# Performance work log

Hardware: AMD Instinct MI355X
Metric: run time of the kernel (lower is better)

The kernel has to match this reference:

```python
import jax, jax.numpy as jnp
import numpy as np

B, S, D, H = 2, 2048, 1024, 16
HD = D // H


def setup_inputs() -> dict:
    key = jax.random.key(0)
    ks = jax.random.split(key, 6)
    std = 1.0 / np.sqrt(D)
    return {
        "hidden_states": jax.random.normal(ks[0], (B, S, D), dtype=jnp.float32),
        "attention_mask": jnp.zeros((B, 1, S, S), dtype=jnp.float32),
        "Wq": jax.random.normal(ks[1], (D, D), dtype=jnp.float32) * std,
        "bq": jnp.zeros((D,), dtype=jnp.float32),
        "Wk": jax.random.normal(ks[2], (D, D), dtype=jnp.float32) * std,
        "bk": jnp.zeros((D,), dtype=jnp.float32),
        "Wv": jax.random.normal(ks[3], (D, D), dtype=jnp.float32) * std,
        "bv": jnp.zeros((D,), dtype=jnp.float32),
        "Wo": jax.random.normal(ks[4], (D, D), dtype=jnp.float32) * std,
        "bo": jnp.zeros((D,), dtype=jnp.float32),
    }


def reference(hidden_states, attention_mask, Wq, bq, Wk, bk, Wv, bv, Wo, bo):
    scale = HD ** (-0.5)
    # torch Linear: y = x @ W^T + b
    def proj(x, W, b):
        y = jnp.einsum('bsd,ed->bse', x, W) + b
        return y.reshape(B, S, H, HD).transpose(0, 2, 1, 3)  # [B,H,S,HD]
    q = proj(hidden_states, Wq, bq)
    k = proj(hidden_states, Wk, bk)
    v = proj(hidden_states, Wv, bv)
    scores = jnp.einsum('bhqd,bhkd->bhqk', q, k) * scale + attention_mask
    attn = jax.nn.softmax(scores, axis=-1)  # dropout p=0.0 -> identity
    out = jnp.einsum('bhqk,bhkd->bhqd', attn, v)
    out = out.transpose(0, 2, 1, 3).reshape(B, S, D)
    return jnp.einsum('bsd,ed->bse', out, Wo) + bo
```

## Files before the change

kernel.cpp:

```cpp
#include <hip/hip_runtime.h>
#include <hip/hip_bf16.h>
#include <stdint.h>

#define Bb 2
#define Ss 2048
#define Dd 1024
#define Hh 16
#define HD 64

typedef __attribute__((ext_vector_type(8))) __bf16 bf16x8;
typedef __attribute__((ext_vector_type(4))) __bf16 bf16x4;
typedef __attribute__((ext_vector_type(2))) __bf16 bf16x2;
typedef __attribute__((ext_vector_type(4))) float f32x4;
typedef __attribute__((ext_vector_type(16))) float f32x16;

#define LOG2E 1.44269504088896f
#define SCL2 (0.125f * LOG2E)

#define HS_N   (Bb * Ss * Dd)
#define W_N    (Dd * Dd)
#define B_N    (Dd)
#define CAN_HS 0
#define CAN_WQ (CAN_HS + HS_N)
#define CAN_BQ (CAN_WQ + W_N)
#define CAN_WK (CAN_BQ + B_N)
#define CAN_BK (CAN_WK + W_N)
#define CAN_WV (CAN_BK + B_N)
#define CAN_BV (CAN_WV + W_N)
#define CAN_WO (CAN_BV + B_N)
#define CAN_BO (CAN_WO + W_N)
#define CAN_END (CAN_BO + B_N)
#define TSZ    (Bb * Hh * Ss * HD)
#define WS_ELEMS (CAN_END + 4 * TSZ)
#define WS_NEED ((size_t)WS_ELEMS * 2)

__device__ __forceinline__ void gl_lds16(const __bf16* g, __bf16* l) {
  __builtin_amdgcn_global_load_lds(
      (const __attribute__((address_space(1))) void*)g,
      (__attribute__((address_space(3))) void*)l,
      16, 0, 0);
}

__device__ __forceinline__ void cfence() { asm volatile("" ::: "memory"); }

__global__ void canon_kernel(const float* hs, const float* Wq, const float* bq,
                             const float* Wk, const float* bk, const float* Wv,
                             const float* bv, const float* Wo, const float* bo,
                             __bf16* __restrict__ dst) {
  const float* srcs[9] = {hs, Wq, bq, Wk, bk, Wv, bv, Wo, bo};
  const long starts[10] = {CAN_HS, CAN_WQ, CAN_BQ, CAN_WK, CAN_BK,
                           CAN_WV, CAN_BV, CAN_WO, CAN_BO, CAN_END};
  const long nchunks = CAN_END / 8;
  for (long c = blockIdx.x * blockDim.x + threadIdx.x; c < nchunks;
       c += (long)gridDim.x * blockDim.x) {
    const long i = c * 8;
    int seg = 0;
#pragma unroll
    for (int t = 1; t < 9; t++) seg += (i >= starts[t]) ? 1 : 0;
    const float* s = srcs[seg] + (i - starts[seg]);
    bf16x8 v;
#pragma unroll
    for (int e = 0; e < 8; e++) v[e] = (__bf16)s[e];
    *(bf16x8*)(dst + i) = v;
  }
}

template <int MODE, typename OutT>
__global__ __launch_bounds__(256, 2) void gemm_bt(
    const __bf16* __restrict__ A,
    const __bf16* __restrict__ W0, const __bf16* __restrict__ W1,
    const __bf16* __restrict__ W2,
    const __bf16* __restrict__ b0, const __bf16* __restrict__ b1,
    const __bf16* __restrict__ b2,
    OutT* __restrict__ O0, OutT* __restrict__ O1, OutT* __restrict__ O2) {
  __shared__ __align__(16) __bf16 sA[128 * 32 + 12544];
  __shared__ __align__(16) __bf16 sB[128 * 32];
  const int tid = threadIdx.x;
  const int lane = tid & 63;
  const int wid = tid >> 6;
  const int quad = lane >> 4;
  const int l15 = lane & 15;
  const int mBlock = blockIdx.x * 128;

  const __bf16* W;
  const __bf16* bias;
  OutT* Out;
  int nBlock, which = 0;
  if (MODE == 0) {
    which = blockIdx.y >> 3;
    nBlock = (blockIdx.y & 7) * 128;
    W = which == 0 ? W0 : (which == 1 ? W1 : W2);
    bias = which == 0 ? b0 : (which == 1 ? b1 : b2);
    Out = which == 0 ? O0 : (which == 1 ? O1 : O2);
  } else {
    nBlock = blockIdx.y * 128;
    W = W0;
    bias = b0;
    Out = O0;
  }

  const int waveM = (wid >> 1) * 64;
  const int waveN = (wid & 1) * 64;

  f32x4 acc[4][4] = {};

  const int c1 = wid * 64 + lane;
  const int c2 = c1 + 256;
  const __bf16* Ar1 = A + (mBlock + (c1 >> 2)) * Dd + (c1 & 3) * 8;
  const __bf16* Ar2 = A + (mBlock + (c2 >> 2)) * Dd + (c2 & 3) * 8;
  const __bf16* Wr1 = W + (nBlock + (c1 >> 2)) * Dd + (c1 & 3) * 8;
  const __bf16* Wr2 = W + (nBlock + (c2 >> 2)) * Dd + (c2 & 3) * 8;
  __bf16* ldsA1 = sA + (wid * 64) * 8;
  __bf16* ldsA2 = sA + (wid * 64 + 256) * 8;
  __bf16* ldsB1 = sB + (wid * 64) * 8;
  __bf16* ldsB2 = sB + (wid * 64 + 256) * 8;

  for (int k0 = 0; k0 < Dd; k0 += 32) {
    gl_lds16(Ar1 + k0, ldsA1);
    gl_lds16(Ar2 + k0, ldsA2);
    gl_lds16(Wr1 + k0, ldsB1);
    gl_lds16(Wr2 + k0, ldsB2);
    __syncthreads();

    bf16x8 aF[4], bF[4];
#pragma unroll
    for (int mi = 0; mi < 4; mi++)
      aF[mi] = *(const bf16x8*)(sA + (waveM + mi * 16 + l15) * 32 + quad * 8);
#pragma unroll
    for (int ni = 0; ni < 4; ni++)
      bF[ni] = *(const bf16x8*)(sB + (waveN + ni * 16 + l15) * 32 + quad * 8);
#pragma unroll
    for (int mi = 0; mi < 4; mi++)
#pragma unroll
      for (int ni = 0; ni < 4; ni++)
        acc[mi][ni] = __builtin_amdgcn_mfma_f32_16x16x32_bf16(
            aF[mi], bF[ni], acc[mi][ni], 0, 0, 0);
    __syncthreads();
  }

#pragma unroll
  for (int ni = 0; ni < 4; ni++) {
    const int ng = nBlock + waveN + ni * 16 + l15;
    const float bv = (float)bias[ng];
#pragma unroll
    for (int mi = 0; mi < 4; mi++) {
      const int mg0 = mBlock + waveM + mi * 16 + quad * 4;
      if (MODE == 0 && which == 2) {
        const int b = mg0 >> 11, s0 = mg0 & 2047;
        const int h = ng >> 6, hd = ng & 63;
        bf16x4 pk;
#pragma unroll
        for (int r = 0; r < 4; r++) pk[r] = (__bf16)(acc[mi][ni][r] + bv);
        *(bf16x4*)((__bf16*)Out + (((b * Hh + h) * HD + hd) * Ss) + s0) = pk;
      } else {
#pragma unroll
        for (int r = 0; r < 4; r++) {
          float v = acc[mi][ni][r] + bv;
          const int m = mg0 + r;
          if (MODE == 0) {
            if (which == 0) v *= SCL2;
            const int b = m >> 11, s = m & 2047;
            const int h = ng >> 6, hd = ng & 63;
            Out[(((b * Hh + h) * Ss + s) * HD) + hd] = (OutT)v;
          } else {
            Out[m * Dd + ng] = (OutT)v;
          }
        }
      }
    }
  }
}

__global__ __launch_bounds__(256, 4) void attn_fused(
    const __bf16* __restrict__ Qg, const __bf16* __restrict__ Kg,
    const __bf16* __restrict__ Vt, const float* __restrict__ Mf,
    __bf16* __restrict__ Og) {
  __shared__ __align__(16) union {
    __bf16 buf[2][9216];
    struct {
      float O[2][64][32];
      float L[2][32];
    } m;
  } sh;

  const int tid = threadIdx.x;
  const int lane = tid & 63;
  const int wid = tid >> 6;
  const int qg = wid & 1;
  const int kvh = wid >> 1;
  const int l31 = lane & 31;
  const int hi = lane >> 5;
  const int bh = blockIdx.y;
  const int b = bh >> 4;
  const int h = bh & 15;
  const int qw = blockIdx.x * 64 + qg * 32 + l31;

  const __bf16* Qp = Qg + (size_t)bh * Ss * HD;
  const __bf16* Kp = Kg + (size_t)bh * Ss * HD;
  const __bf16* Vp = Vt + (size_t)bh * HD * Ss;
  const float* Mrow = Mf + ((size_t)b * Ss + qw) * Ss + 32 * kvh + 4 * hi;

  bf16x8 qf[4];
#pragma unroll
  for (int k = 0; k < 4; k++)
    qf[k] = *(const bf16x8*)(Qp + (size_t)qw * HD + k * 16 + hi * 8);

  const int cA = tid, cB = 256 + tid;
#define STAGE_KV(BI, KVS)                                                     \
  {                                                                           \
    const int rwA = (cA & 255) >> 2, rwB = (cB & 255) >> 2;                   \
    const int slA = (cA & 3) ^ ((rwA >> 1) & 3);                              \
    const int slB = (cB & 3) ^ ((rwB >> 1) & 3);                              \
    __bf16* kb = sh.buf[BI];                                                  \
    gl_lds16(Kp + ((KVS) + rwA) * HD + (cA >> 8) * 32 + slA * 8, kb + cA * 8);\
    gl_lds16(Kp + ((KVS) + rwB) * HD + (cB >> 8) * 32 + slB * 8, kb + cB * 8);\
    __bf16* vb = sh.buf[BI] + 4096;                                           \
    gl_lds16(Vp + (size_t)rwA * Ss + (KVS) + (cA >> 8) * 32 + slA * 8,        \
             vb + cA * 8);                                                    \
    gl_lds16(Vp + (size_t)rwB * Ss + (KVS) + (cB >> 8) * 32 + slB * 8,        \
             vb + cB * 8);                                                    \
  }

  f32x16 o[2] = {};
  f32x4 lacc = {0.f, 0.f, 0.f, 0.f};

  const int rsw = (l31 >> 1) & 3;

  STAGE_KV(0, 0);
  f32x4 mcur[4], mnext[4];
#pragma unroll
  for (int g = 0; g < 4; g++) mcur[g] = *(const f32x4*)(Mrow + g * 8);

  for (int it = 0; it < 32; ++it) {
    const int bufc = it & 1;
    cfence();
    asm volatile("s_waitcnt vmcnt(0)" ::: "memory");
    cfence();
    __builtin_amdgcn_s_barrier();
    cfence();
    if (it < 31) {
      STAGE_KV(bufc ^ 1, (it + 1) * 64);
      cfence();
#pragma unroll
      for (int g = 0; g < 4; g++)
        mnext[g] = *(const f32x4*)(Mrow + (it + 1) * 64 + g * 8);
      cfence();
    }

    f32x16 sacc;
#pragma unroll
    for (int g = 0; g < 4; g++)
#pragma unroll
      for (int r = 0; r < 4; r++) sacc[g * 4 + r] = mcur[g][r] * LOG2E;
    __builtin_amdgcn_s_setprio(1);
#pragma unroll
    for (int k = 0; k < 4; k++) {
      const int ps = (((k & 1) << 1) | hi) ^ rsw;
      bf16x8 kf = *(const bf16x8*)(sh.buf[bufc] +
                                   ((k >> 1) * 64 + kvh * 32 + l31) * 32 +
                                   ps * 8);
      sacc = __builtin_amdgcn_mfma_f32_32x32x16_bf16(kf, qf[k], sacc, 0, 0, 0);
    }
    __builtin_amdgcn_s_setprio(0);

    f32x4 sv[4];
#pragma unroll
    for (int g = 0; g < 4; g++)
#pragma unroll
      for (int r = 0; r < 4; r++)
        sv[g][r] = __builtin_amdgcn_exp2f(sacc[g * 4 + r]);
    lacc += (sv[0] + sv[1]) + (sv[2] + sv[3]);

    bf16x4 pk[4];
#pragma unroll
    for (int g = 0; g < 4; g++)
#pragma unroll
      for (int r = 0; r < 4; r++) pk[g][r] = (__bf16)sv[g][r];
    union pu { bf16x4 v; uint32_t w[2]; };
    pu s0, s1, r0, r1;
    s0.v = hi ? pk[0] : pk[1];
    s1.v = hi ? pk[2] : pk[3];
    r0.w[0] = __shfl_xor((int)s0.w[0], 32);
    r0.w[1] = __shfl_xor((int)s0.w[1], 32);
    r1.w[0] = __shfl_xor((int)s1.w[0], 32);
    r1.w[1] = __shfl_xor((int)s1.w[1], 32);
    bf16x8 pf[2];
    {
      bf16x4 lo0 = hi ? r0.v : pk[0], hi0 = hi ? pk[1] : r0.v;
      bf16x4 lo1 = hi ? r1.v : pk[2], hi1 = hi ? pk[3] : r1.v;
#pragma unroll
      for (int e = 0; e < 4; e++) {
        pf[0][e] = lo0[e]; pf[0][e + 4] = hi0[e];
        pf[1][e] = lo1[e]; pf[1][e + 4] = hi1[e];
      }
    }

    __builtin_amdgcn_s_setprio(1);
#pragma unroll
    for (int k = 0; k < 2; k++)
#pragma unroll
      for (int hb = 0; hb < 2; hb++) {
        const int ps = ((k << 1) | hi) ^ rsw;
        bf16x8 vf = *(const bf16x8*)(sh.buf[bufc] + 4096 +
                                     (kvh * 64 + hb * 32 + l31) * 32 +
                                     ps * 8);
        o[hb] = __builtin_amdgcn_mfma_f32_32x32x16_bf16(vf, pf[k], o[hb],
                                                        0, 0, 0);
      }
    __builtin_amdgcn_s_setprio(0);

#pragma unroll
    for (int g = 0; g < 4; g++) mcur[g] = mnext[g];
  }

  float l = lacc[0] + lacc[1] + lacc[2] + lacc[3];
  l += __shfl_xor(l, 32);

  __syncthreads();
  if (kvh == 1) {
#pragma unroll
    for (int hb = 0; hb < 2; hb++)
#pragma unroll
      for (int r = 0; r < 16; r++) {
        const int hd = hb * 32 + (r & 3) + 8 * (r >> 2) + 4 * hi;
        sh.m.O[qg][hd][l31] = o[hb][r];
      }
    if (hi == 0) sh.m.L[qg][l31] = l;
  }
  __syncthreads();
  if (kvh == 0) {
#pragma unroll
    for (int hb = 0; hb < 2; hb++)
#pragma unroll
      for (int r = 0; r < 16; r++) {
        const int hd = hb * 32 + (r & 3) + 8 * (r >> 2) + 4 * hi;
        o[hb][r] += sh.m.O[qg][hd][l31];
      }
    l += sh.m.L[qg][l31];
    const float inv = 1.0f / l;
    __bf16* Ow = Og + (((size_t)b * Ss + qw) * Hh + h) * HD;
#pragma unroll
    for (int hb = 0; hb < 2; hb++)
#pragma unroll
      for (int g = 0; g < 4; g++) {
        const int hd = hb * 32 + g * 8 + 4 * hi;
        bf16x2 w0, w1;
        w0[0] = (__bf16)(o[hb][g * 4 + 0] * inv);
        w0[1] = (__bf16)(o[hb][g * 4 + 1] * inv);
        w1[0] = (__bf16)(o[hb][g * 4 + 2] * inv);
        w1[1] = (__bf16)(o[hb][g * 4 + 3] * inv);
        *(bf16x2*)(Ow + hd) = w0;
        *(bf16x2*)(Ow + hd + 2) = w1;
      }
  }
}

extern "C" void kernel_launch(void* const* d_in, const int* in_sizes, int n_in,
                              void* d_out, int out_size, void* d_ws,
                              size_t ws_size, hipStream_t stream) {
  if (ws_size < WS_NEED) return;

  __bf16* ws = (__bf16*)d_ws;
  const __bf16* hsC = ws + CAN_HS;
  const __bf16* WqC = ws + CAN_WQ;
  const __bf16* bqC = ws + CAN_BQ;
  const __bf16* WkC = ws + CAN_WK;
  const __bf16* bkC = ws + CAN_BK;
  const __bf16* WvC = ws + CAN_WV;
  const __bf16* bvC = ws + CAN_BV;
  const __bf16* WoC = ws + CAN_WO;
  const __bf16* boC = ws + CAN_BO;
  __bf16* Q = ws + CAN_END;
  __bf16* K = Q + TSZ;
  __bf16* V = K + TSZ;
  __bf16* AW = V + TSZ;
  float* out = (float*)d_out;

  canon_kernel<<<2048, 256, 0, stream>>>(
      (const float*)d_in[0], (const float*)d_in[2], (const float*)d_in[3],
      (const float*)d_in[4], (const float*)d_in[5], (const float*)d_in[6],
      (const float*)d_in[7], (const float*)d_in[8], (const float*)d_in[9], ws);
  gemm_bt<0, __bf16><<<dim3(32, 24), 256, 0, stream>>>(
      hsC, WqC, WkC, WvC, bqC, bkC, bvC, Q, K, V);
  attn_fused<<<dim3(32, 32), 256, 0, stream>>>(Q, K, V, (const float*)d_in[1],
                                               AW);
  gemm_bt<1, float><<<dim3(32, 8), 256, 0, stream>>>(
      AW, WoC, WoC, WoC, boC, boC, boC, out, out, out);
}
```

Before: 257.2 us.

## Stage attention mask tiles through LDS via direct global-to-LDS loads

The attention mask is no longer read per-thread from global memory into registers with a one-tile prefetch. Each 64x64 fp32 mask tile is now loaded cooperatively with global_load_lds into a swizzled shared buffer, then read back from LDS. The aim is coalesced mask reads and fewer VGPRs spent holding prefetched mask values. The cost is a second barrier per iteration, a single (not double) mask buffer that serialises load and use, and 16KB more LDS, which lowers the launch-bounds occupancy hint from 4 to 3 blocks.

```diff
diff --git a/kernel.cpp b/kernel.cpp
--- a/kernel.cpp
+++ b/kernel.cpp
@@ -41,6 +41,13 @@
       16, 0, 0);
 }
 
+__device__ __forceinline__ void gl_lds16f(const float* g, float* l) {
+  __builtin_amdgcn_global_load_lds(
+      (const __attribute__((address_space(1))) void*)g,
+      (__attribute__((address_space(3))) void*)l,
+      16, 0, 0);
+}
+
 __device__ __forceinline__ void cfence() { asm volatile("" ::: "memory"); }
 
 __global__ void canon_kernel(const float* hs, const float* Wq, const float* bq,
@@ -171,12 +178,15 @@
   }
 }
 
-__global__ __launch_bounds__(256, 4) void attn_fused(
+__global__ __launch_bounds__(256, 3) void attn_fused(
     const __bf16* __restrict__ Qg, const __bf16* __restrict__ Kg,
     const __bf16* __restrict__ Vt, const float* __restrict__ Mf,
     __bf16* __restrict__ Og) {
   __shared__ __align__(16) union {
-    __bf16 buf[2][9216];
+    struct {
+      __bf16 kv[2][8192];
+      float mk[64 * 64];
+    } s;
     struct {
       float O[2][64][32];
       float L[2][32];
@@ -193,12 +203,13 @@
   const int bh = blockIdx.y;
   const int b = bh >> 4;
   const int h = bh & 15;
-  const int qw = blockIdx.x * 64 + qg * 32 + l31;
+  const int qb0 = blockIdx.x * 64;
+  const int qw = qb0 + qg * 32 + l31;
 
   const __bf16* Qp = Qg + (size_t)bh * Ss * HD;
   const __bf16* Kp = Kg + (size_t)bh * Ss * HD;
   const __bf16* Vp = Vt + (size_t)bh * HD * Ss;
-  const float* Mrow = Mf + ((size_t)b * Ss + qw) * Ss + 32 * kvh + 4 * hi;
+  const float* Mp = Mf + (size_t)b * Ss * Ss;
 
   bf16x8 qf[4];
 #pragma unroll
@@ -211,25 +222,35 @@
     const int rwA = (cA & 255) >> 2, rwB = (cB & 255) >> 2;                   \
     const int slA = (cA & 3) ^ ((rwA >> 1) & 3);                              \
     const int slB = (cB & 3) ^ ((rwB >> 1) & 3);                              \
-    __bf16* kb = sh.buf[BI];                                                  \
+    __bf16* kb = sh.s.kv[BI];                                                 \
     gl_lds16(Kp + ((KVS) + rwA) * HD + (cA >> 8) * 32 + slA * 8, kb + cA * 8);\
     gl_lds16(Kp + ((KVS) + rwB) * HD + (cB >> 8) * 32 + slB * 8, kb + cB * 8);\
-    __bf16* vb = sh.buf[BI] + 4096;                                           \
+    __bf16* vb = sh.s.kv[BI] + 4096;                                          \
     gl_lds16(Vp + (size_t)rwA * Ss + (KVS) + (cA >> 8) * 32 + slA * 8,        \
              vb + cA * 8);                                                    \
     gl_lds16(Vp + (size_t)rwB * Ss + (KVS) + (cB >> 8) * 32 + slB * 8,        \
              vb + cB * 8);                                                    \
   }
 
+#define STAGE_M(KVS)                                                          \
+  {                                                                           \
+    _Pragma("unroll")                                                         \
+    for (int rr = 0; rr < 4; rr++) {                                          \
+      const int c = tid + rr * 256;                                           \
+      const int mq = c >> 4;                                                  \
+      const int kvi = ((c & 15) ^ (mq & 7)) * 4;                              \
+      gl_lds16f(Mp + (size_t)(qb0 + mq) * Ss + (KVS) + kvi,                   \
+                sh.s.mk + c * 4);                                             \
+    }                                                                         \
+  }
+
   f32x16 o[2] = {};
   f32x4 lacc = {0.f, 0.f, 0.f, 0.f};
 
   const int rsw = (l31 >> 1) & 3;
 
   STAGE_KV(0, 0);
-  f32x4 mcur[4], mnext[4];
-#pragma unroll
-  for (int g = 0; g < 4; g++) mcur[g] = *(const f32x4*)(Mrow + g * 8);
+  STAGE_M(0);
 
   for (int it = 0; it < 32; ++it) {
     const int bufc = it & 1;
@@ -241,9 +262,22 @@
     if (it < 31) {
       STAGE_KV(bufc ^ 1, (it + 1) * 64);
       cfence();
-#pragma unroll
-      for (int g = 0; g < 4; g++)
-        mnext[g] = *(const f32x4*)(Mrow + (it + 1) * 64 + g * 8);
+    }
+
+    f32x4 mc[4];
+    const int mq = qg * 32 + l31;
+#pragma unroll
+    for (int g = 0; g < 4; g++) {
+      const int p16 = (8 * kvh + 2 * g + hi) ^ (l31 & 7);
+      mc[g] = *(const f32x4*)(sh.s.mk + mq * 64 + p16 * 4);
+    }
+    cfence();
+    asm volatile("s_waitcnt lgkmcnt(0)" ::: "memory");
+    cfence();
+    __builtin_amdgcn_s_barrier();
+    cfence();
+    if (it < 31) {
+      STAGE_M((it + 1) * 64);
       cfence();
     }
 
@@ -251,12 +285,12 @@
 #pragma unroll
     for (int g = 0; g < 4; g++)
 #pragma unroll
-      for (int r = 0; r < 4; r++) sacc[g * 4 + r] = mcur[g][r] * LOG2E;
+      for (int r = 0; r < 4; r++) sacc[g * 4 + r] = mc[g][r] * LOG2E;
     __builtin_amdgcn_s_setprio(1);
 #pragma unroll
     for (int k = 0; k < 4; k++) {
       const int ps = (((k & 1) << 1) | hi) ^ rsw;
-      bf16x8 kf = *(const bf16x8*)(sh.buf[bufc] +
+      bf16x8 kf = *(const bf16x8*)(sh.s.kv[bufc] +
                                    ((k >> 1) * 64 + kvh * 32 + l31) * 32 +
                                    ps * 8);
       sacc = __builtin_amdgcn_mfma_f32_32x32x16_bf16(kf, qf[k], sacc, 0, 0, 0);
@@ -301,16 +335,13 @@
 #pragma unroll
       for (int hb = 0; hb < 2; hb++) {
         const int ps = ((k << 1) | hi) ^ rsw;
-        bf16x8 vf = *(const bf16x8*)(sh.buf[bufc] + 4096 +
+        bf16x8 vf = *(const bf16x8*)(sh.s.kv[bufc] + 4096 +
                                      (kvh * 64 + hb * 32 + l31) * 32 +
                                      ps * 8);
         o[hb] = __builtin_amdgcn_mfma_f32_32x32x16_bf16(vf, pf[k], o[hb],
                                                         0, 0, 0);
       }
     __builtin_amdgcn_s_setprio(0);
-
-#pragma unroll
-    for (int g = 0; g < 4; g++) mcur[g] = mnext[g];
   }
 
   float l = lacc[0] + lacc[1] + lacc[2] + lacc[3];
```

Measured after the change: 236.3 us. 1.09x faster.
